# Performance work log

Measured on AMD Instinct MI355X. Metric: run time of the kernel, lower is better.

## Reference

```python
import jax, jax.numpy as jnp
import numpy as np

RADIUS = 3
DIAM = 2 * RADIUS + 1  # 7
NP = DIAM * DIAM       # 49 taps


def _cubic(d, a=-0.75):
    # torch bicubic kernel (a = -0.75)
    d = np.abs(d)
    return np.where(d <= 1, (a + 2) * d**3 - (a + 3) * d**2 + 1,
                    np.where(d < 2, a * d**3 - 5 * a * d**2 + 8 * a * d - 4 * a, 0.0))


def _resize_matrix(out_size, in_size):
    # dense [out,in] matrix reproducing torch F.interpolate bicubic, align_corners=False
    i = np.arange(out_size)
    x = (i + 0.5) * in_size / out_size - 0.5
    x0 = np.floor(x).astype(np.int64)
    t = x - x0
    W = np.zeros((out_size, in_size), np.float32)
    for k in range(-1, 3):
        w = _cubic(t - k)
        idx = np.clip(x0 + k, 0, in_size - 1)  # border replicate
        np.add.at(W, (i, idx), w.astype(np.float32))
    return jnp.asarray(W)


def _bicubic(x, GH, GW):
    B, C, H, W = x.shape
    Wh = _resize_matrix(GH, H)
    Ww = _resize_matrix(GW, W)
    return jnp.einsum('Hh,bchw,Ww->bcHW', Wh, x, Ww)


def _jbu(source, guidance, w1, b1, w2, b2, temp, sigma):
    # FeatUp JBULearnedRange.forward (eval mode: Dropout2d is identity)
    B, _, GH, GW = guidance.shape
    # range_proj: 1x1 conv -> GELU -> 1x1 conv
    q = jnp.einsum('kc,bchw->bkhw', w1, guidance) + b1[None, :, None, None]
    q = jax.nn.gelu(q, approximate=False)
    q = jnp.einsum('kc,bchw->bkhw', w2, q) + b2[None, :, None, None]  # [B,32,GH,GW]
    qp = jnp.pad(q, ((0, 0), (0, 0), (RADIUS, RADIUS), (RADIUS, RADIUS)), mode='reflect')
    # scores[b,p,h,w] = <key at center, key at offset p> (avoids B*32*49*H*W unfold)
    scores = jnp.stack([jnp.sum(qp[:, :, di:di + GH, dj:dj + GW] * q, axis=1)
                        for di in range(DIAM) for dj in range(DIAM)], axis=1)  # [B,49,GH,GW]
    t = jnp.clip(jnp.exp(temp), 1e-4, 1e4)
    range_kernel = jax.nn.softmax(t * scores, axis=1)
    dist = jnp.linspace(-1.0, 1.0, DIAM)
    gy, gx = jnp.meshgrid(dist, dist, indexing='ij')
    spatial_kernel = jnp.exp(-(gy**2 + gx**2) / (2.0 * sigma**2)).reshape(1, NP, 1, 1)
    k = range_kernel * spatial_kernel
    k = k / jnp.clip(jnp.sum(k, axis=1, keepdims=True), 1e-7, None)
    hr = _bicubic(source, GH, GW)
    hrp = jnp.pad(hr, ((0, 0), (0, 0), (RADIUS, RADIUS), (RADIUS, RADIUS)), mode='reflect')
    # AdaptiveConv: per-pixel 7x7 kernel applied to all channels
    out = jnp.zeros_like(hr)
    p_idx = 0
    for di in range(DIAM):
        for dj in range(DIAM):
            out = out + hrp[:, :, di:di + GH, dj:dj + GW] * k[:, p_idx][:, None]
            p_idx += 1
    return out


def _forward(x, guidance, linear_w, linear_b, w1s, b1s, w2s, b2s, temps, sigmas):
    f = (x @ linear_w.T + linear_b).reshape(-1, 3, 18, 18)
    for i in range(4):  # up1..up4, each fed the FULL guidance as in the Decoder
        f = _jbu(f, guidance, w1s[i], b1s[i], w2s[i], b2s[i], temps[i], sigmas[i])
    return f


def setup_inputs() -> dict:
    key = jax.random.key(0)
    ks = jax.random.split(key, 6)
    B = 8
    return {
        'x': jax.random.normal(ks[0], (B, 1000), jnp.float32),
        'guidance': jax.random.uniform(ks[1], (B, 3, 224, 224), jnp.float32),
        'linear_w': jax.random.normal(ks[2], (972, 1000), jnp.float32) * 0.03,
        'linear_b': jnp.zeros((972,), jnp.float32),
        'w1s': jax.random.normal(ks[3], (4, 32, 3), jnp.float32) * 0.1,
        'b1s': jnp.zeros((4, 32), jnp.float32),
        'w2s': jax.random.normal(ks[4], (4, 32, 32), jnp.float32) * 0.1,
        'b2s': jnp.zeros((4, 32), jnp.float32),
        'temps': jnp.zeros((4,), jnp.float32),   # range_temp init 0.0
        'sigmas': jnp.ones((4,), jnp.float32),   # sigma_spatial init 1.0
    }


def reference(x, guidance, linear_w, linear_b, w1s, b1s, w2s, b2s, temps, sigmas):
    return _forward(x, guidance, linear_w, linear_b, w1s, b1s, w2s, b2s, temps, sigmas)
```

## Files before the change

### kernel.cpp

```cpp
#include <hip/hip_runtime.h>
#include <hip/hip_fp16.h>
#include <math.h>

#define GHH 224
#define GWW 224
#define HW (GHH*GWW)
#define BATCH 8
#define RAD 3
#define DIAM 7
#define QC 32
#define TILE 16
#define TP (TILE + 2*RAD)
#define TPIX (TP*TP)
#define CS 485
#define SQ_B 31040

typedef _Float16 h2 __attribute__((ext_vector_type(2)));
typedef _Float16 v8h __attribute__((ext_vector_type(8)));
typedef float v4f __attribute__((ext_vector_type(4)));

#if defined(__has_builtin)
#if __has_builtin(__builtin_amdgcn_fdot2)
#define HAS_FDOT2 1
#endif
#endif

__device__ __forceinline__ h2 as_h2(float f) { union { float f; h2 h; } u; u.f = f; return u.h; }

__device__ __forceinline__ float dot2acc(float a, float b, float acc) {
#ifdef HAS_FDOT2
    return __builtin_amdgcn_fdot2(as_h2(a), as_h2(b), acc, false);
#else
    union { float f; __half2 h; } ua, ub; ua.f = a; ub.f = b;
    float2 fa = __half22float2(ua.h), fb = __half22float2(ub.h);
    return acc + fa.x * fb.x + fa.y * fb.y;
#endif
}

__device__ __forceinline__ float dot16(const float4& a, const float4& b, float acc) {
    acc = dot2acc(a.x, b.x, acc);
    acc = dot2acc(a.y, b.y, acc);
    acc = dot2acc(a.z, b.z, acc);
    acc = dot2acc(a.w, b.w, acc);
    return acc;
}

__device__ __forceinline__ int refl(int i) {
    if (i < 0) i = -i;
    if (i >= GHH) i = 2 * GHH - 2 - i;
    return i;
}

__device__ __forceinline__ float gelu_fast(float v) {
    float u = 0.7978845608f * v * (1.f + 0.044715f * v * v);
    float e = __expf(2.f * u);
    float th = 1.f - 2.f / (e + 1.f);
    return 0.5f * v * (1.f + th);
}

__global__ void linear_prep_kernel(const float* __restrict__ x,
                                   const float* __restrict__ W,
                                   const float* __restrict__ bias,
                                   float* __restrict__ f0,
                                   const float* __restrict__ w2s,
                                   __half* __restrict__ wsB,
                                   const float* __restrict__ w1s,
                                   const float* __restrict__ b1s,
                                   __half* __restrict__ wsW1,
                                   const float* __restrict__ guid,
                                   float4* __restrict__ guid4) {
    int blk = blockIdx.x;
    if (blk >= 1946) {
        int i = (blk - 1946) * 256 + threadIdx.x;
        int b = i / HW, pix = i % HW;
        guid4[i] = make_float4(guid[(b * 3) * HW + pix],
                               guid[(b * 3 + 1) * HW + pix],
                               guid[(b * 3 + 2) * HW + pix], 0.f);
        return;
    }
    if (blk == 1945) {
        int tid = threadIdx.x;
        if (tid < 128) {
            int s = tid >> 5, c = tid & 31;
            wsW1[tid * 4 + 0] = __float2half(w1s[s * 96 + c * 3 + 0]);
            wsW1[tid * 4 + 1] = __float2half(w1s[s * 96 + c * 3 + 1]);
            wsW1[tid * 4 + 2] = __float2half(w1s[s * 96 + c * 3 + 2]);
            wsW1[tid * 4 + 3] = __float2half(b1s[s * 32 + c]);
        }
        return;
    }
    if (blk == 1944) {
        int tid = threadIdx.x;
        int s = tid >> 6, l = tid & 63;
        int n0 = l & 15, kq = l >> 4;
        const float* w2 = w2s + s * 1024;
        __half* dst = wsB + (size_t)tid * 16;
        #pragma unroll
        for (int j = 0; j < 8; j++) {
            dst[j]     = __float2half(w2[n0 * QC + kq * 8 + j]);
            dst[8 + j] = __float2half(w2[(n0 + 16) * QC + kq * 8 + j]);
        }
        return;
    }
    int gwave = (blk * blockDim.x + threadIdx.x) >> 6;
    int lane = threadIdx.x & 63;
    if (gwave >= BATCH * 972) return;
    int b = gwave / 972, j = gwave % 972;
    const float* xr = x + b * 1000;
    const float* wr = W + j * 1000;
    float s = 0.f;
    for (int k = lane; k < 1000; k += 64)
        s += xr[k] * wr[k];
    #pragma unroll
    for (int off = 32; off; off >>= 1) s += __shfl_down(s, off, 64);
    if (lane == 0) f0[gwave] = s + bias[j];
}

__device__ __forceinline__ float cubicw(float d) {
    d = fabsf(d);
    if (d <= 1.f) return ((1.25f * d - 2.25f) * d) * d + 1.f;
    if (d < 2.f)  return ((-0.75f * d + 3.75f) * d - 6.f) * d + 3.f;
    return 0.f;
}

__global__ void bicubic_kernel(const float* __restrict__ f0, float4* __restrict__ hr4) {
    int idx = blockIdx.x * blockDim.x + threadIdx.x;
    if (idx >= BATCH * HW) return;
    int pix = idx % HW;
    int b = idx / HW;
    int w = pix % GWW, h = pix / GWW;
    float xx = (w + 0.5f) * (18.f / 224.f) - 0.5f;
    float yy = (h + 0.5f) * (18.f / 224.f) - 0.5f;
    float fx0 = floorf(xx), fy0 = floorf(yy);
    int x0 = (int)fx0, y0 = (int)fy0;
    float tx = xx - fx0, ty = yy - fy0;
    float wx[4], wy[4];
    int ix[4], iy[4];
    #pragma unroll
    for (int k = 0; k < 4; k++) {
        wx[k] = cubicw(tx - (float)(k - 1));
        wy[k] = cubicw(ty - (float)(k - 1));
        int a = x0 + (k - 1); ix[k] = min(max(a, 0), 17);
        a = y0 + (k - 1);     iy[k] = min(max(a, 0), 17);
    }
    float acc[3];
    #pragma unroll
    for (int c = 0; c < 3; c++) {
        const float* src = f0 + (b * 3 + c) * 324;
        float a = 0.f;
        #pragma unroll
        for (int ky = 0; ky < 4; ky++) {
            float rowv = 0.f;
            #pragma unroll
            for (int kx = 0; kx < 4; kx++) rowv += wx[kx] * src[iy[ky] * 18 + ix[kx]];
            a += wy[ky] * rowv;
        }
        acc[c] = a;
    }
    hr4[idx] = make_float4(acc[0], acc[1], acc[2], 0.f);
}

__global__ __launch_bounds__(256, 4) void jbu_kernel(
    const float4* __restrict__ guid4,
    const __half* __restrict__ wsW1,
    const __half* __restrict__ wsB, const float* __restrict__ b2,
    const float4* __restrict__ hr4,
    float4* __restrict__ out4,
    float* __restrict__ outP,
    const float* __restrict__ temps,
    const float* __restrict__ sigmas,
    int stage)
{
    __shared__ __align__(16) char smem[SQ_B + TPIX * 16];
    float4* sq = (float4*)smem;
    float4* sh = (float4*)(smem + SQ_B);

    const int tx = threadIdx.x, ty = threadIdx.y;
    const int tid = ty * TILE + tx;
    const int b = blockIdx.z;
    const int h0 = blockIdx.y * TILE, w0 = blockIdx.x * TILE;

    const bool interior = (h0 >= RAD) && (h0 + TILE + RAD <= GHH) &&
                          (w0 >= RAD) && (w0 + TILE + RAD <= GWW);
    if (interior) {
        const float4* hb = hr4 + (size_t)b * HW + (size_t)(h0 - RAD) * GWW + (w0 - RAD);
        for (int i = tid; i < TPIX; i += 256) {
            int r = i / TP, cx = i % TP;
            sh[i] = hb[(size_t)r * GWW + cx];
        }
    } else {
        for (int i = tid; i < TPIX; i += 256) {
            int r = i / TP, cx = i % TP;
            int gh = refl(h0 - RAD + r);
            int gw = refl(w0 - RAD + cx);
            sh[i] = hr4[(size_t)b * HW + (size_t)gh * GWW + gw];
        }
    }

    const int w = tid >> 6, l = tid & 63;
    const int n0 = l & 15, kq = l >> 4;
    const v8h* Bp = (const v8h*)(wsB + ((size_t)stage * 64 + l) * 16);
    const v8h W2a = Bp[0], W2b = Bp[1];
    const float4 b2a = *(const float4*)(b2 + 4 * kq);
    const float4 b2b = *(const float4*)(b2 + 16 + 4 * kq);
    union { _Float16 h[32]; float4 f4[4]; } W1;
    {
        const float4* wp = (const float4*)(wsW1 + stage * 128 + kq * 32);
        W1.f4[0] = wp[0]; W1.f4[1] = wp[1]; W1.f4[2] = wp[2]; W1.f4[3] = wp[3];
    }
    const int plane0 = kq >> 1;
    const int boff   = (kq & 1) * 8;

    #pragma unroll 1
    for (int r2 = 0; r2 < 2; r2++) {
        #pragma unroll
        for (int tt = 0; tt < 4; tt++) {
            int base = r2 * 256 + w * 64 + tt * 16;
            int p = base + n0;
            int pc = min(p, TPIX - 1);
            int rr = pc / TP, cc = pc - rr * TP;
            int gh = refl(h0 - RAD + rr), gw = refl(w0 - RAD + cc);
            float4 g = guid4[(size_t)b * HW + (size_t)gh * GWW + gw];
            union { _Float16 h[8]; v8h v; } A;
            #pragma unroll
            for (int j = 0; j < 8; j++) {
                float vv = fmaf((float)W1.h[j * 4], g.x,
                           fmaf((float)W1.h[j * 4 + 1], g.y,
                           fmaf((float)W1.h[j * 4 + 2], g.z, (float)W1.h[j * 4 + 3])));
                A.h[j] = (_Float16)gelu_fast(vv);
            }
            v4f D0 = {0.f, 0.f, 0.f, 0.f}, D1 = {0.f, 0.f, 0.f, 0.f};
            D0 = __builtin_amdgcn_mfma_f32_16x16x32_f16(W2a, A.v, D0, 0, 0, 0);
            D1 = __builtin_amdgcn_mfma_f32_16x16x32_f16(W2b, A.v, D1, 0, 0, 0);
            if (p < TPIX) {
                union { _Float16 h[4]; uint2 u; } q0, q1;
                q0.h[0] = (_Float16)(D0[0] + b2a.x);
                q0.h[1] = (_Float16)(D0[1] + b2a.y);
                q0.h[2] = (_Float16)(D0[2] + b2a.z);
                q0.h[3] = (_Float16)(D0[3] + b2a.w);
                q1.h[0] = (_Float16)(D1[0] + b2b.x);
                q1.h[1] = (_Float16)(D1[1] + b2b.y);
                q1.h[2] = (_Float16)(D1[2] + b2b.z);
                q1.h[3] = (_Float16)(D1[3] + b2b.w);
                *(uint2*)(smem + (plane0 * CS + p) * 16 + boff)       = q0.u;
                *(uint2*)(smem + ((2 + plane0) * CS + p) * 16 + boff) = q1.u;
            }
        }
    }
    __syncthreads();

    int ci = (ty + RAD) * TP + tx + RAD;
    float4 c0 = sq[ci], c1 = sq[CS + ci], c2 = sq[2 * CS + ci], c3 = sq[3 * CS + ci];

    float t = __expf(temps[stage]);
    t = fminf(fmaxf(t, 1e-4f), 1e4f);
    float sig = sigmas[stage];
    float inv2s2 = 1.f / (2.f * sig * sig);
    float sd[DIAM];
    #pragma unroll
    for (int i = 0; i < DIAM; i++) {
        float d = (float)(i - 3) * (1.f / 3.f);
        sd[i] = __expf(-d * d * inv2s2);
    }

    float es = 0.f, wsum = 0.f, o0 = 0.f, o1 = 0.f, o2 = 0.f;
    #pragma unroll
    for (int di = 0; di < DIAM; di++) {
        int rb = (ty + di) * TP + tx;
        float sy = sd[di];
        #pragma unroll
        for (int dj = 0; dj < DIAM; dj++) {
            int ni = rb + dj;
            float s = dot16(c0, sq[ni], 0.f);
            s = dot16(c1, sq[CS + ni], s);
            s = dot16(c2, sq[2 * CS + ni], s);
            s = dot16(c3, sq[3 * CS + ni], s);
            float4 hv = sh[ni];
            float e = __expf(t * s);
            float wgt = e * sy * sd[dj];
            es += e; wsum += wgt;
            o0 += wgt * hv.x; o1 += wgt * hv.y; o2 += wgt * hv.z;
        }
    }
    float rk = 1.f / fmaxf(wsum, 1e-7f * es);

    if (stage < 3) {
        out4[(size_t)b * HW + (size_t)(h0 + ty) * GWW + (w0 + tx)] =
            make_float4(o0 * rk, o1 * rk, o2 * rk, 0.f);
    } else {
        size_t obase = (size_t)b * 3 * HW + (size_t)(h0 + ty) * GWW + (w0 + tx);
        outP[obase]          = o0 * rk;
        outP[obase + HW]     = o1 * rk;
        outP[obase + 2 * HW] = o2 * rk;
    }
}

extern "C" void kernel_launch(void* const* d_in, const int* in_sizes, int n_in,
                              void* d_out, int out_size, void* d_ws, size_t ws_size,
                              hipStream_t stream) {
    const float* x      = (const float*)d_in[0];
    const float* guid   = (const float*)d_in[1];
    const float* lw     = (const float*)d_in[2];
    const float* lb     = (const float*)d_in[3];
    const float* w1s    = (const float*)d_in[4];
    const float* b1s    = (const float*)d_in[5];
    const float* w2s    = (const float*)d_in[6];
    const float* b2s    = (const float*)d_in[7];
    const float* temps  = (const float*)d_in[8];
    const float* sigmas = (const float*)d_in[9];

    char* ws = (char*)d_ws;
    const size_t P4_BYTES = (size_t)BATCH * HW * sizeof(float4);
    float4* guid4 = (float4*)ws;
    float4* hr4A  = (float4*)(ws + P4_BYTES);
    float4* hr4B  = (float4*)(ws + 2 * P4_BYTES);
    float*  f0    = (float*)(ws + 3 * P4_BYTES);
    __half* wsB   = (__half*)(ws + 3 * P4_BYTES + 31104);
    __half* wsW1  = (__half*)(ws + 3 * P4_BYTES + 31104 + 8192);

    linear_prep_kernel<<<1946 + 1568, 256, 0, stream>>>(
        x, lw, lb, f0, w2s, wsB, w1s, b1s, wsW1, guid, guid4);
    bicubic_kernel<<<(BATCH * HW + 255) / 256, 256, 0, stream>>>(f0, hr4A);

    dim3 jgrid(14, 14, BATCH), jblock(16, 16);
    const float4* hins[4]  = { hr4A, hr4B, hr4A, hr4B };
    float4*       fouts[4] = { hr4B, hr4A, hr4B, nullptr };
    for (int s = 0; s < 4; s++) {
        jbu_kernel<<<jgrid, jblock, 0, stream>>>(
            guid4, wsW1, wsB, b2s + s * 32,
            hins[s], fouts[s], (s == 3) ? (float*)d_out : nullptr,
            temps, sigmas, s);
    }
}
```

Before: 279.5 us.

## Compute two horizontal pixels per thread with swizzled shared-memory layout

Halves the JBU block to 128 threads so that each thread produces two horizontally adjacent output pixels. The 8 neighbour columns each thread loads are shared between the two pixels' 7x7 windows, which cuts shared-memory loads per output. Shared-memory columns are swizzled into even/odd halves so that stride-2 accesses across threads avoid bank conflicts. The cost is more registers per thread and fewer threads per block, which may lower occupancy and latency hiding. The q-projection prologue is reshaped to match the smaller block.

```diff
diff --git a/kernel.cpp b/kernel.cpp
--- a/kernel.cpp
+++ b/kernel.cpp
@@ -50,6 +50,8 @@
     if (i >= GHH) i = 2 * GHH - 2 - i;
     return i;
 }
+
+__device__ __forceinline__ int swz(int c) { return (c >> 1) + (c & 1) * 11; }
 
 __device__ __forceinline__ float gelu_fast(float v) {
     float u = 0.7978845608f * v * (1.f + 0.044715f * v * v);
@@ -160,7 +162,7 @@
     hr4[idx] = make_float4(acc[0], acc[1], acc[2], 0.f);
 }
 
-__global__ __launch_bounds__(256, 4) void jbu_kernel(
+__global__ __launch_bounds__(128, 4) void jbu_kernel(
     const float4* __restrict__ guid4,
     const __half* __restrict__ wsW1,
     const __half* __restrict__ wsB, const float* __restrict__ b2,
@@ -175,8 +177,9 @@
     float4* sq = (float4*)smem;
     float4* sh = (float4*)(smem + SQ_B);
 
-    const int tx = threadIdx.x, ty = threadIdx.y;
-    const int tid = ty * TILE + tx;
+    const int tx = threadIdx.x;
+    const int ty = threadIdx.y;
+    const int tid = ty * 8 + tx;
     const int b = blockIdx.z;
     const int h0 = blockIdx.y * TILE, w0 = blockIdx.x * TILE;
 
@@ -184,16 +187,16 @@
                           (w0 >= RAD) && (w0 + TILE + RAD <= GWW);
     if (interior) {
         const float4* hb = hr4 + (size_t)b * HW + (size_t)(h0 - RAD) * GWW + (w0 - RAD);
-        for (int i = tid; i < TPIX; i += 256) {
+        for (int i = tid; i < TPIX; i += 128) {
             int r = i / TP, cx = i % TP;
-            sh[i] = hb[(size_t)r * GWW + cx];
+            sh[r * TP + swz(cx)] = hb[(size_t)r * GWW + cx];
         }
     } else {
-        for (int i = tid; i < TPIX; i += 256) {
+        for (int i = tid; i < TPIX; i += 128) {
             int r = i / TP, cx = i % TP;
             int gh = refl(h0 - RAD + r);
             int gw = refl(w0 - RAD + cx);
-            sh[i] = hr4[(size_t)b * HW + (size_t)gh * GWW + gw];
+            sh[r * TP + swz(cx)] = hr4[(size_t)b * HW + (size_t)gh * GWW + gw];
         }
     }
 
@@ -212,45 +215,58 @@
     const int boff   = (kq & 1) * 8;
 
     #pragma unroll 1
-    for (int r2 = 0; r2 < 2; r2++) {
-        #pragma unroll
-        for (int tt = 0; tt < 4; tt++) {
-            int base = r2 * 256 + w * 64 + tt * 16;
-            int p = base + n0;
-            int pc = min(p, TPIX - 1);
-            int rr = pc / TP, cc = pc - rr * TP;
-            int gh = refl(h0 - RAD + rr), gw = refl(w0 - RAD + cc);
-            float4 g = guid4[(size_t)b * HW + (size_t)gh * GWW + gw];
-            union { _Float16 h[8]; v8h v; } A;
+    for (int r2 = 0; r2 < 4; r2++) {
+        #pragma unroll
+        for (int tt = 0; tt < 2; tt++) {
+            int base = (r2 * 2 + w) * 64 + tt * 32 + 0;
             #pragma unroll
-            for (int j = 0; j < 8; j++) {
-                float vv = fmaf((float)W1.h[j * 4], g.x,
-                           fmaf((float)W1.h[j * 4 + 1], g.y,
-                           fmaf((float)W1.h[j * 4 + 2], g.z, (float)W1.h[j * 4 + 3])));
-                A.h[j] = (_Float16)gelu_fast(vv);
+            for (int uu = 0; uu < 2; uu++) {
+                int bb = base + uu * 16;
+                int p = bb + n0;
+                int pc = min(p, TPIX - 1);
+                int rr = pc / TP, cc = pc - rr * TP;
+                int gh = refl(h0 - RAD + rr), gw = refl(w0 - RAD + cc);
+                float4 g = guid4[(size_t)b * HW + (size_t)gh * GWW + gw];
+                union { _Float16 h[8]; v8h v; } A;
+                #pragma unroll
+                for (int j = 0; j < 8; j++) {
+                    float vv = fmaf((float)W1.h[j * 4], g.x,
+                               fmaf((float)W1.h[j * 4 + 1], g.y,
+                               fmaf((float)W1.h[j * 4 + 2], g.z, (float)W1.h[j * 4 + 3])));
+                    A.h[j] = (_Float16)gelu_fast(vv);
+                }
+                v4f D0 = {0.f, 0.f, 0.f, 0.f}, D1 = {0.f, 0.f, 0.f, 0.f};
+                D0 = __builtin_amdgcn_mfma_f32_16x16x32_f16(W2a, A.v, D0, 0, 0, 0);
+                D1 = __builtin_amdgcn_mfma_f32_16x16x32_f16(W2b, A.v, D1, 0, 0, 0);
+                if (p < TPIX) {
+                    int rr2 = p / TP, cc2 = p - rr2 * TP;
+                    int slot = rr2 * TP + swz(cc2);
+                    union { _Float16 h[4]; uint2 u; } q0, q1;
+                    q0.h[0] = (_Float16)(D0[0] + b2a.x);
+                    q0.h[1] = (_Float16)(D0[1] + b2a.y);
+                    q0.h[2] = (_Float16)(D0[2] + b2a.z);
+                    q0.h[3] = (_Float16)(D0[3] + b2a.w);
+                    q1.h[0] = (_Float16)(D1[0] + b2b.x);
+                    q1.h[1] = (_Float16)(D1[1] + b2b.y);
+                    q1.h[2] = (_Float16)(D1[2] + b2b.z);
+                    q1.h[3] = (_Float16)(D1[3] + b2b.w);
+                    *(uint2*)(smem + (plane0 * CS + slot) * 16 + boff)       = q0.u;
+                    *(uint2*)(smem + ((2 + plane0) * CS + slot) * 16 + boff) = q1.u;
+                }
             }
-            v4f D0 = {0.f, 0.f, 0.f, 0.f}, D1 = {0.f, 0.f, 0.f, 0.f};
-            D0 = __builtin_amdgcn_mfma_f32_16x16x32_f16(W2a, A.v, D0, 0, 0, 0);
-            D1 = __builtin_amdgcn_mfma_f32_16x16x32_f16(W2b, A.v, D1, 0, 0, 0);
-            if (p < TPIX) {
-                union { _Float16 h[4]; uint2 u; } q0, q1;
-                q0.h[0] = (_Float16)(D0[0] + b2a.x);
-                q0.h[1] = (_Float16)(D0[1] + b2a.y);
-                q0.h[2] = (_Float16)(D0[2] + b2a.z);
-                q0.h[3] = (_Float16)(D0[3] + b2a.w);
-                q1.h[0] = (_Float16)(D1[0] + b2b.x);
-                q1.h[1] = (_Float16)(D1[1] + b2b.y);
-                q1.h[2] = (_Float16)(D1[2] + b2b.z);
-                q1.h[3] = (_Float16)(D1[3] + b2b.w);
-                *(uint2*)(smem + (plane0 * CS + p) * 16 + boff)       = q0.u;
-                *(uint2*)(smem + ((2 + plane0) * CS + p) * 16 + boff) = q1.u;
-            }
         }
     }
     __syncthreads();
 
-    int ci = (ty + RAD) * TP + tx + RAD;
-    float4 c0 = sq[ci], c1 = sq[CS + ci], c2 = sq[2 * CS + ci], c3 = sq[3 * CS + ci];
+    float4 A0c[4], A1c[4];
+    {
+        int rbc = (ty + RAD) * TP;
+        #pragma unroll
+        for (int c = 0; c < 4; c++) {
+            A0c[c] = sq[c * CS + rbc + tx + 12];
+            A1c[c] = sq[c * CS + rbc + tx + 2];
+        }
+    }
 
     float t = __expf(temps[stage]);
     t = fminf(fmaxf(t, 1e-4f), 1e4f);
@@ -263,35 +279,52 @@
         sd[i] = __expf(-d * d * inv2s2);
     }
 
-    float es = 0.f, wsum = 0.f, o0 = 0.f, o1 = 0.f, o2 = 0.f;
+    float es0 = 0.f, ws0 = 0.f, n00 = 0.f, n01 = 0.f, n02 = 0.f;
+    float es1 = 0.f, ws1 = 0.f, n10 = 0.f, n11 = 0.f, n12 = 0.f;
     #pragma unroll
     for (int di = 0; di < DIAM; di++) {
-        int rb = (ty + di) * TP + tx;
-        float sy = sd[di];
-        #pragma unroll
-        for (int dj = 0; dj < DIAM; dj++) {
-            int ni = rb + dj;
-            float s = dot16(c0, sq[ni], 0.f);
-            s = dot16(c1, sq[CS + ni], s);
-            s = dot16(c2, sq[2 * CS + ni], s);
-            s = dot16(c3, sq[3 * CS + ni], s);
+        const int rb = (ty + di) * TP + tx;
+        const float sy = sd[di];
+        #pragma unroll
+        for (int dj = 0; dj < 8; dj++) {
+            const int SOFF = (dj >> 1) + (dj & 1) * 11;
+            const int ni = rb + SOFF;
+            float4 v0 = sq[ni], v1 = sq[CS + ni], v2 = sq[2 * CS + ni], v3 = sq[3 * CS + ni];
             float4 hv = sh[ni];
-            float e = __expf(t * s);
-            float wgt = e * sy * sd[dj];
-            es += e; wsum += wgt;
-            o0 += wgt * hv.x; o1 += wgt * hv.y; o2 += wgt * hv.z;
-        }
-    }
-    float rk = 1.f / fmaxf(wsum, 1e-7f * es);
+            if (dj < 7) {
+                float s = dot16(A0c[0], v0, 0.f);
+                s = dot16(A0c[1], v1, s);
+                s = dot16(A0c[2], v2, s);
+                s = dot16(A0c[3], v3, s);
+                float e = __expf(t * s);
+                float wgt = e * sy * sd[dj];
+                es0 += e; ws0 += wgt;
+                n00 += wgt * hv.x; n01 += wgt * hv.y; n02 += wgt * hv.z;
+            }
+            if (dj > 0) {
+                float s = dot16(A1c[0], v0, 0.f);
+                s = dot16(A1c[1], v1, s);
+                s = dot16(A1c[2], v2, s);
+                s = dot16(A1c[3], v3, s);
+                float e = __expf(t * s);
+                float wgt = e * sy * sd[dj - 1];
+                es1 += e; ws1 += wgt;
+                n10 += wgt * hv.x; n11 += wgt * hv.y; n12 += wgt * hv.z;
+            }
+        }
+    }
+    float r0 = 1.f / fmaxf(ws0, 1e-7f * es0);
+    float r1 = 1.f / fmaxf(ws1, 1e-7f * es1);
 
     if (stage < 3) {
-        out4[(size_t)b * HW + (size_t)(h0 + ty) * GWW + (w0 + tx)] =
-            make_float4(o0 * rk, o1 * rk, o2 * rk, 0.f);
+        size_t obase = (size_t)b * HW + (size_t)(h0 + ty) * GWW + (w0 + 2 * tx);
+        out4[obase]     = make_float4(n00 * r0, n01 * r0, n02 * r0, 0.f);
+        out4[obase + 1] = make_float4(n10 * r1, n11 * r1, n12 * r1, 0.f);
     } else {
-        size_t obase = (size_t)b * 3 * HW + (size_t)(h0 + ty) * GWW + (w0 + tx);
-        outP[obase]          = o0 * rk;
-        outP[obase + HW]     = o1 * rk;
-        outP[obase + 2 * HW] = o2 * rk;
+        size_t obase = (size_t)b * 3 * HW + (size_t)(h0 + ty) * GWW + (w0 + 2 * tx);
+        *(float2*)&outP[obase]          = make_float2(n00 * r0, n10 * r1);
+        *(float2*)&outP[obase + HW]     = make_float2(n01 * r0, n11 * r1);
+        *(float2*)&outP[obase + 2 * HW] = make_float2(n02 * r0, n12 * r1);
     }
 }
 
@@ -322,7 +355,7 @@
         x, lw, lb, f0, w2s, wsB, w1s, b1s, wsW1, guid, guid4);
     bicubic_kernel<<<(BATCH * HW + 255) / 256, 256, 0, stream>>>(f0, hr4A);
 
-    dim3 jgrid(14, 14, BATCH), jblock(16, 16);
+    dim3 jgrid(14, 14, BATCH), jblock(8, 16);
     const float4* hins[4]  = { hr4A, hr4B, hr4A, hr4B };
     float4*       fouts[4] = { hr4B, hr4A, hr4B, nullptr };
     for (int s = 0; s < 4; s++) {
```

After: 349.1 us. 24.9% more time.
